# Performance work log

Hardware: AMD Instinct MI355X
Metric: run time of the kernel (lower is better)

The kernel has to match this reference:

```python
import jax, jax.numpy as jnp
import numpy as np


def setup_inputs() -> dict:
    key = jax.random.key(0)
    k_x, k_g, k_fc, k_pj = jax.random.split(key, 4)
    B, T, C, H, E = 4, 2048, 1024, 2048, 8
    n_layer = 12
    x = jax.random.normal(k_x, (B, T, C), dtype=jnp.float32)
    w_gate = 0.02 * jax.random.normal(k_g, (C, E), dtype=jnp.float32)
    w_fc = 0.02 * jax.random.normal(k_fc, (C, H, E), dtype=jnp.float32)
    w_proj = (0.02 * (2 * n_layer) ** -0.5) * jax.random.normal(k_pj, (H, C, E), dtype=jnp.float32)
    return {"x": x, "w_gate": w_gate, "w_fc": w_fc, "w_proj": w_proj, "top_k": 2}


def reference(x, w_gate, w_fc, w_proj, top_k):
    # x: (B,T,C); w_gate: (C,E); w_fc: (C,H,E); w_proj: (H,C,E)
    E = w_gate.shape[-1]
    gate = jnp.einsum('btc,ce->bte', x, w_gate)                  # gating logits
    top_vals, top_idx = jax.lax.top_k(gate, top_k)               # (B,T,K) — raw logits used as combine weights (as in source)
    # Per-expert combine weight: sum_k top_val_k * onehot(idx_k) — zero for unselected experts.
    # This is mathematically identical to gathering the K expert weight slices per token
    # (the source's gather+einsum) but avoids the (B,T,C,H,K) weight blowup.
    onehot = jax.nn.one_hot(top_idx, E, dtype=x.dtype)           # (B,T,K,E)
    w_e = jnp.einsum('btk,btke->bte', top_vals, onehot)          # (B,T,E)
    h = jax.nn.silu(jnp.einsum('btc,che->bthe', x, w_fc))        # (B,T,H,E)
    o = jnp.einsum('bthe,bte,hce->btc', h, w_e, w_proj)          # weighted expert combine
    return o
```

## Files before the change

### kernel.cpp

```cpp
#include <hip/hip_runtime.h>
#include <hip/hip_bf16.h>


#define NTOK 8192
#define CD   1024
#define HD   2048
#define NE   8
#define NSLOT 16384
#define MTILES 20
#define BK   64
#define NT1  (CD / BK)
#define NT2  (HD / BK)
#define PACK_BLOCKS 2048

typedef short  short4_t  __attribute__((ext_vector_type(4)));
typedef short  short8_t  __attribute__((ext_vector_type(8)));
typedef __bf16 bf16x8_t  __attribute__((ext_vector_type(8)));
typedef float  f32x4_t   __attribute__((ext_vector_type(4)));

struct FragArg {
  short8_t v;
  __device__ operator short8_t() const { return v; }
  __device__ operator bf16x8_t() const { return __builtin_bit_cast(bf16x8_t, v); }
};

static __device__ __forceinline__ float b2f(unsigned short u) {
  union { float f; unsigned int i; } w; w.i = ((unsigned int)u) << 16; return w.f;
}
static __device__ __forceinline__ unsigned short f2b(float f) {
  unsigned int u = __float_as_uint(f);
  u += 0x7fffu + ((u >> 16) & 1u);
  return (unsigned short)(u >> 16);
}
static __device__ __forceinline__ void gl2lds16(const void* g, void* l) {
  __builtin_amdgcn_global_load_lds((__attribute__((address_space(1))) void*)g,
                                   (__attribute__((address_space(3))) void*)l,
                                   16, 0, 0);
}

static __device__ __forceinline__ void pack_tile(
    const float* __restrict__ in, unsigned short* __restrict__ out,
    int D0, int D1, int b0, int b1, unsigned short* smem, int t)
{
  int d1i = t & 31, d0q = t >> 5;
  #pragma unroll
  for (int r = 0; r < 4; ++r) {
    int d0i = d0q * 4 + r;
    const float* src = in + ((size_t)(b0 + d0i) * D1 + (b1 + d1i)) * NE;
    float4 v0 = *(const float4*)src;
    float4 v1 = *(const float4*)(src + 4);
    unsigned short* dst0 = &smem[d1i * 40 + d0i];
    dst0[0 * 32 * 40] = f2b(v0.x);
    dst0[1 * 32 * 40] = f2b(v0.y);
    dst0[2 * 32 * 40] = f2b(v0.z);
    dst0[3 * 32 * 40] = f2b(v0.w);
    dst0[4 * 32 * 40] = f2b(v1.x);
    dst0[5 * 32 * 40] = f2b(v1.y);
    dst0[6 * 32 * 40] = f2b(v1.z);
    dst0[7 * 32 * 40] = f2b(v1.w);
  }
  __syncthreads();
  int dchunk = t & 3, d1w = (t >> 2) & 31, ehalf = t >> 7;
  #pragma unroll
  for (int p = 0; p < 4; ++p) {
    int e = ehalf + 2 * p;
    short8_t v = *(const short8_t*)&smem[e * 32 * 40 + d1w * 40 + dchunk * 8];
    *(short8_t*)(out + ((size_t)e * D1 + (b1 + d1w)) * D0 + b0 + dchunk * 8) = v;
  }
}

#define GATE_BLOCKS (NTOK / 4)
__global__ __launch_bounds__(256) void prep_kernel(
    const float* __restrict__ x, const float* __restrict__ wg,
    const float* __restrict__ wfc,
    unsigned short* __restrict__ xb, unsigned short* __restrict__ wfcp,
    int* __restrict__ tok_e, float* __restrict__ tok_v,
    int* __restrict__ g_counts)
{
  __shared__ __align__(16) unsigned short lds[NE * 32 * 40];
  __shared__ int hist[NE];
  int t = threadIdx.x;

  if (blockIdx.x < GATE_BLOCKS) {
    if (t < NE) hist[t] = 0;
    __syncthreads();
    int wv = t >> 6, lane = t & 63;
    int tk = blockIdx.x * 4 + wv;
    const float* xr = x + (size_t)tk * CD;
    unsigned short* xbr = xb + (size_t)tk * CD;
    float acc[NE] = {0, 0, 0, 0, 0, 0, 0, 0};
    #pragma unroll
    for (int jj = 0; jj < 4; ++jj) {
      int c0 = (lane + 64 * jj) * 4;
      float4 xv = *(const float4*)(xr + c0);
      short4_t ob;
      ob[0] = (short)f2b(xv.x); ob[1] = (short)f2b(xv.y);
      ob[2] = (short)f2b(xv.z); ob[3] = (short)f2b(xv.w);
      *(short4_t*)(xbr + c0) = ob;
      #pragma unroll
      for (int j = 0; j < 4; ++j) {
        float xf = (j == 0) ? xv.x : (j == 1) ? xv.y : (j == 2) ? xv.z : xv.w;
        const float* wr = wg + (size_t)(c0 + j) * NE;
        float4 w0 = *(const float4*)wr;
        float4 w1 = *(const float4*)(wr + 4);
        acc[0] += xf * w0.x; acc[1] += xf * w0.y;
        acc[2] += xf * w0.z; acc[3] += xf * w0.w;
        acc[4] += xf * w1.x; acc[5] += xf * w1.y;
        acc[6] += xf * w1.z; acc[7] += xf * w1.w;
      }
    }
    #pragma unroll
    for (int off = 32; off >= 1; off >>= 1)
      #pragma unroll
      for (int e = 0; e < NE; ++e) acc[e] += __shfl_down(acc[e], off, 64);
    if (lane == 0) {
      float v1 = -3.0e38f, v2 = -3.0e38f; int i1 = 0, i2 = 1;
      #pragma unroll
      for (int e = 0; e < NE; ++e) {
        float g = acc[e];
        if (g > v1) { v2 = v1; i2 = i1; v1 = g; i1 = e; }
        else if (g > v2) { v2 = g; i2 = e; }
      }
      tok_e[tk * 2] = i1; tok_e[tk * 2 + 1] = i2;
      tok_v[tk * 2] = v1; tok_v[tk * 2 + 1] = v2;
      atomicAdd(&hist[i1], 1); atomicAdd(&hist[i2], 1);
    }
    __syncthreads();
    if (t < NE && hist[t] > 0) atomicAdd(&g_counts[t], hist[t]);
  } else {
    int pid = blockIdx.x - GATE_BLOCKS;
    int bx = pid & 63, by = pid >> 6;
    pack_tile(wfc, wfcp, CD, HD, by * 32, bx * 32, lds, t);
  }
}

__global__ __launch_bounds__(256) void scatter_kernel(
    const int* __restrict__ tok_e, const float* __restrict__ tok_v,
    const int* __restrict__ g_counts, int* __restrict__ g_cursor,
    int* __restrict__ g_base,
    int* __restrict__ bucket_tok, float* __restrict__ bucket_v,
    int* __restrict__ slot_of)
{
  int gid = blockIdx.x * 256 + threadIdx.x;
  int lane = threadIdx.x & 63;
  int base[NE];
  { int o = 0;
    #pragma unroll
    for (int e = 0; e < NE; ++e) { base[e] = o; o += g_counts[e]; } }
  int e = tok_e[gid];
  unsigned long long lanebit = 1ull << lane;
  int pos = 0;
  #pragma unroll
  for (int ee = 0; ee < NE; ++ee) {
    unsigned long long m = __ballot(e == ee);
    if (e == ee) {
      int leader = __ffsll((long long)m) - 1;
      int cnt = __popcll(m);
      int start = 0;
      if (lane == leader) start = atomicAdd(&g_cursor[ee], cnt);
      start = __shfl(start, leader, 64);
      pos = start + __popcll(m & (lanebit - 1));
    }
  }
  int sl = base[e] + pos;
  bucket_tok[sl] = gid >> 1;
  bucket_v[sl]   = tok_v[gid];
  slot_of[gid]   = sl;
  if (gid < NE) g_base[gid] = base[gid];
}

__global__ __launch_bounds__(256, 2) void gemm1_kernel(
    const unsigned short* __restrict__ xb, const unsigned short* __restrict__ wfcp,
    const float* __restrict__ wpj, unsigned short* __restrict__ wpjp,
    const int* __restrict__ g_counts, const int* __restrict__ g_base,
    const int* __restrict__ bucket_tok, const float* __restrict__ bucket_v,
    unsigned short* __restrict__ hbuf)
{
  __shared__ __align__(16) unsigned short smem[2][2][2][128][32];
  __shared__ int   s_tok[128];
  __shared__ float s_v[128];
  int t = threadIdx.x;

  if (blockIdx.x < PACK_BLOCKS) {
    int pid = blockIdx.x;
    int bx = pid & 63, by = pid >> 6;
    pack_tile(wpj, wpjp, HD, CD, bx * 32, by * 32, &smem[0][0][0][0][0], t);
    return;
  }

  int id = blockIdx.x - PACK_BLOCKS;
  int e = id & 7;
  int r = id >> 3;
  int nt = r & 15;
  int mt = r >> 4;

  int cnt = g_counts[e];
  int m0 = mt * 128;
  if (m0 >= cnt) return;
  int base = g_base[e];
  int n0 = nt * 128;

  if (t < 128) {
    int ok = (m0 + t) < cnt;
    s_tok[t] = ok ? bucket_tok[base + m0 + t] : 0;
    s_v[t]   = ok ? bucket_v[base + m0 + t] : 0.0f;
  }
  __syncthreads();

  int lane = t & 63, wv = t >> 6;
  int srow = t >> 2;
  int spc  = t & 3;
  int sw   = (spc ^ (srow & 3)) * 8;
  const unsigned short* aS0 = xb + (size_t)s_tok[srow] * CD + sw;
  const unsigned short* aS1 = xb + (size_t)s_tok[srow + 64] * CD + sw;
  const unsigned short* bS0 = wfcp + ((size_t)e * HD + n0 + srow) * CD + sw;
  const unsigned short* bS1 = wfcp + ((size_t)e * HD + n0 + srow + 64) * CD + sw;

  #define STG1(tt, kh) do {                                              \
    int _ko = (tt) * BK + (kh) * 32;                                     \
    int _b  = (tt) & 1;                                                  \
    gl2lds16(aS0 + _ko, &smem[0][_b][kh][wv * 16][0]);                   \
    gl2lds16(aS1 + _ko, &smem[0][_b][kh][64 + wv * 16][0]);              \
    gl2lds16(bS0 + _ko, &smem[1][_b][kh][wv * 16][0]);                   \
    gl2lds16(bS1 + _ko, &smem[1][_b][kh][64 + wv * 16][0]);              \
  } while (0)

  int wm = (wv & 1) * 64, wn = (wv >> 1) * 64;
  int ml = lane & 15, kq = lane >> 4;
  int sw8 = (kq ^ (ml & 3)) * 8;

  f32x4_t acc[4][4];
  #pragma unroll
  for (int i = 0; i < 4; ++i)
    #pragma unroll
    for (int j = 0; j < 4; ++j) acc[i][j] = (f32x4_t){0.f, 0.f, 0.f, 0.f};

  STG1(0, 0); STG1(0, 1); STG1(1, 0);
  asm volatile("s_waitcnt vmcnt(8)" ::: "memory");
  __builtin_amdgcn_s_barrier();
  asm volatile("" ::: "memory");

  #pragma unroll 1
  for (int tt = 0; tt < NT1; ++tt) {
    int buf = tt & 1;
    short8_t af[4], bfr[4];
    #pragma unroll
    for (int i = 0; i < 4; ++i) {
      af[i]  = *(const short8_t*)&smem[0][buf][0][wm + i * 16 + ml][sw8];
      bfr[i] = *(const short8_t*)&smem[1][buf][0][wn + i * 16 + ml][sw8];
    }
    if (tt + 1 < NT1) STG1(tt + 1, 1);
    __builtin_amdgcn_s_barrier();
    __builtin_amdgcn_s_setprio(1);
    #pragma unroll
    for (int i = 0; i < 4; ++i)
      #pragma unroll
      for (int j = 0; j < 4; ++j)
        acc[i][j] = __builtin_amdgcn_mfma_f32_16x16x32_bf16(
            FragArg{af[i]}, FragArg{bfr[j]}, acc[i][j], 0, 0, 0);
    __builtin_amdgcn_s_setprio(0);
    if (tt < NT1 - 1) asm volatile("s_waitcnt vmcnt(8)" ::: "memory");
    else              asm volatile("s_waitcnt vmcnt(0)" ::: "memory");
    __builtin_amdgcn_s_barrier();
    asm volatile("" ::: "memory");
    #pragma unroll
    for (int i = 0; i < 4; ++i) {
      af[i]  = *(const short8_t*)&smem[0][buf][1][wm + i * 16 + ml][sw8];
      bfr[i] = *(const short8_t*)&smem[1][buf][1][wn + i * 16 + ml][sw8];
    }
    if (tt + 2 < NT1) STG1(tt + 2, 0);
    __builtin_amdgcn_s_barrier();
    __builtin_amdgcn_s_setprio(1);
    #pragma unroll
    for (int i = 0; i < 4; ++i)
      #pragma unroll
      for (int j = 0; j < 4; ++j)
        acc[i][j] = __builtin_amdgcn_mfma_f32_16x16x32_bf16(
            FragArg{af[i]}, FragArg{bfr[j]}, acc[i][j], 0, 0, 0);
    __builtin_amdgcn_s_setprio(0);
    if (tt + 2 < NT1)      asm volatile("s_waitcnt vmcnt(8)" ::: "memory");
    else if (tt + 1 < NT1) asm volatile("s_waitcnt vmcnt(4)" ::: "memory");
    __builtin_amdgcn_s_barrier();
    asm volatile("" ::: "memory");
  }
  #undef STG1

  #pragma unroll
  for (int i = 0; i < 4; ++i) {
    int rb = wm + i * 16 + kq * 4;
    #pragma unroll
    for (int r2 = 0; r2 < 4; ++r2) {
      int row = rb + r2;
      if (m0 + row < cnt) {
        float v = s_v[row];
        size_t ro = (size_t)(base + m0 + row) * HD + n0;
        #pragma unroll
        for (int j = 0; j < 4; ++j) {
          float z = acc[i][j][r2];
          float val = v * (z / (1.0f + __expf(-z)));
          hbuf[ro + wn + j * 16 + ml] = f2b(val);
        }
      }
    }
  }
}

__global__ __launch_bounds__(256, 2) void gemm2_kernel(
    const unsigned short* __restrict__ hbuf, const unsigned short* __restrict__ wpjp,
    const int* __restrict__ g_counts, const int* __restrict__ g_base,
    unsigned short* __restrict__ oslot)
{
  __shared__ __align__(16) unsigned short smem[2][2][2][128][32];

  int id = blockIdx.x;
  int e = id & 7;
  int r = id >> 3;
  int nt = r & 7;
  int mt = r >> 3;

  int cnt = g_counts[e];
  int m0 = mt * 128;
  if (m0 >= cnt) return;
  int base = g_base[e];
  int n0 = nt * 128;

  int t = threadIdx.x;
  int lane = t & 63, wv = t >> 6;
  int srow = t >> 2;
  int spc  = t & 3;
  int sw   = (spc ^ (srow & 3)) * 8;
  const unsigned short* aS0 = hbuf + ((size_t)(base + m0 + srow)) * HD + sw;
  const unsigned short* aS1 = hbuf + ((size_t)(base + m0 + srow + 64)) * HD + sw;
  const unsigned short* bS0 = wpjp + ((size_t)e * CD + n0 + srow) * HD + sw;
  const unsigned short* bS1 = wpjp + ((size_t)e * CD + n0 + srow + 64) * HD + sw;

  #define STG2(tt, kh) do {                                              \
    int _ko = (tt) * BK + (kh) * 32;                                     \
    int _b  = (tt) & 1;                                                  \
    gl2lds16(aS0 + _ko, &smem[0][_b][kh][wv * 16][0]);                   \
    gl2lds16(aS1 + _ko, &smem[0][_b][kh][64 + wv * 16][0]);              \
    gl2lds16(bS0 + _ko, &smem[1][_b][kh][wv * 16][0]);                   \
    gl2lds16(bS1 + _ko, &smem[1][_b][kh][64 + wv * 16][0]);              \
  } while (0)

  int wm = (wv & 1) * 64, wn = (wv >> 1) * 64;
  int ml = lane & 15, kq = lane >> 4;
  int sw8 = (kq ^ (ml & 3)) * 8;

  f32x4_t acc[4][4];
  #pragma unroll
  for (int i = 0; i < 4; ++i)
    #pragma unroll
    for (int j = 0; j < 4; ++j) acc[i][j] = (f32x4_t){0.f, 0.f, 0.f, 0.f};

  asm volatile("s_waitcnt vmcnt(0)" ::: "memory");
  STG2(0, 0); STG2(0, 1); STG2(1, 0);
  asm volatile("s_waitcnt vmcnt(8)" ::: "memory");
  __builtin_amdgcn_s_barrier();
  asm volatile("" ::: "memory");

  #pragma unroll 1
  for (int tt = 0; tt < NT2; ++tt) {
    int buf = tt & 1;
    short8_t af[4], bfr[4];
    #pragma unroll
    for (int i = 0; i < 4; ++i) {
      af[i]  = *(const short8_t*)&smem[0][buf][0][wm + i * 16 + ml][sw8];
      bfr[i] = *(const short8_t*)&smem[1][buf][0][wn + i * 16 + ml][sw8];
    }
    if (tt + 1 < NT2) STG2(tt + 1, 1);
    __builtin_amdgcn_s_barrier();
    __builtin_amdgcn_s_setprio(1);
    #pragma unroll
    for (int i = 0; i < 4; ++i)
      #pragma unroll
      for (int j = 0; j < 4; ++j)
        acc[i][j] = __builtin_amdgcn_mfma_f32_16x16x32_bf16(
            FragArg{af[i]}, FragArg{bfr[j]}, acc[i][j], 0, 0, 0);
    __builtin_amdgcn_s_setprio(0);
    if (tt < NT2 - 1) asm volatile("s_waitcnt vmcnt(8)" ::: "memory");
    else              asm volatile("s_waitcnt vmcnt(0)" ::: "memory");
    __builtin_amdgcn_s_barrier();
    asm volatile("" ::: "memory");
    #pragma unroll
    for (int i = 0; i < 4; ++i) {
      af[i]  = *(const short8_t*)&smem[0][buf][1][wm + i * 16 + ml][sw8];
      bfr[i] = *(const short8_t*)&smem[1][buf][1][wn + i * 16 + ml][sw8];
    }
    if (tt + 2 < NT2) STG2(tt + 2, 0);
    __builtin_amdgcn_s_barrier();
    __builtin_amdgcn_s_setprio(1);
    #pragma unroll
    for (int i = 0; i < 4; ++i)
      #pragma unroll
      for (int j = 0; j < 4; ++j)
        acc[i][j] = __builtin_amdgcn_mfma_f32_16x16x32_bf16(
            FragArg{af[i]}, FragArg{bfr[j]}, acc[i][j], 0, 0, 0);
    __builtin_amdgcn_s_setprio(0);
    if (tt + 2 < NT2)      asm volatile("s_waitcnt vmcnt(8)" ::: "memory");
    else if (tt + 1 < NT2) asm volatile("s_waitcnt vmcnt(4)" ::: "memory");
    __builtin_amdgcn_s_barrier();
    asm volatile("" ::: "memory");
  }
  #undef STG2

  #pragma unroll
  for (int i = 0; i < 4; ++i) {
    int rb = wm + i * 16 + kq * 4;
    #pragma unroll
    for (int r2 = 0; r2 < 4; ++r2) {
      int row = rb + r2;
      if (m0 + row < cnt) {
        size_t ro = (size_t)(base + m0 + row) * CD + n0;
        #pragma unroll
        for (int j = 0; j < 4; ++j)
          oslot[ro + wn + j * 16 + ml] = f2b(acc[i][j][r2]);
      }
    }
  }
}

__global__ __launch_bounds__(256) void combine_kernel(
    const unsigned short* __restrict__ oslot, const int* __restrict__ slot_of,
    float* __restrict__ out)
{
  int gid = blockIdx.x * 256 + threadIdx.x;
  int tk = gid >> 7;
  int ch = (gid & 127) * 8;
  int s0 = slot_of[tk * 2], s1 = slot_of[tk * 2 + 1];
  short8_t a = *(const short8_t*)(oslot + (size_t)s0 * CD + ch);
  short8_t b = *(const short8_t*)(oslot + (size_t)s1 * CD + ch);
  float* op = out + (size_t)tk * CD + ch;
  float4 o0, o1;
  o0.x = b2f((unsigned short)a[0]) + b2f((unsigned short)b[0]);
  o0.y = b2f((unsigned short)a[1]) + b2f((unsigned short)b[1]);
  o0.z = b2f((unsigned short)a[2]) + b2f((unsigned short)b[2]);
  o0.w = b2f((unsigned short)a[3]) + b2f((unsigned short)b[3]);
  o1.x = b2f((unsigned short)a[4]) + b2f((unsigned short)b[4]);
  o1.y = b2f((unsigned short)a[5]) + b2f((unsigned short)b[5]);
  o1.z = b2f((unsigned short)a[6]) + b2f((unsigned short)b[6]);
  o1.w = b2f((unsigned short)a[7]) + b2f((unsigned short)b[7]);
  *(float4*)op = o0;
  *(float4*)(op + 4) = o1;
}

extern "C" void kernel_launch(void* const* d_in, const int* in_sizes, int n_in,
                              void* d_out, int out_size, void* d_ws, size_t ws_size,
                              hipStream_t stream)
{
  const float* x   = (const float*)d_in[0];
  const float* wg  = (const float*)d_in[1];
  const float* wfc = (const float*)d_in[2];
  const float* wpj = (const float*)d_in[3];
  float* out = (float*)d_out;

  char* w = (char*)d_ws;
  unsigned short* wfcp  = (unsigned short*)w; w += (size_t)NE * HD * CD * 2;
  unsigned short* wpjp  = (unsigned short*)w; w += (size_t)NE * CD * HD * 2;
  unsigned short* xb    = (unsigned short*)w; w += (size_t)NTOK * CD * 2;
  unsigned short* hbuf  = (unsigned short*)w; w += (size_t)NSLOT * HD * 2;
  unsigned short* oslot = (unsigned short*)w; w += (size_t)NSLOT * CD * 2;
  int*   tok_e      = (int*)w;   w += NSLOT * 4;
  float* tok_v      = (float*)w; w += NSLOT * 4;
  int*   slot_of    = (int*)w;   w += NSLOT * 4;
  int*   bucket_tok = (int*)w;   w += NSLOT * 4;
  float* bucket_v   = (float*)w; w += NSLOT * 4;
  int*   g_counts   = (int*)w;   w += NE * 4;
  int*   g_cursor   = (int*)w;   w += NE * 4;
  int*   g_base     = (int*)w;   w += 256;

  hipMemsetAsync(g_counts, 0, 2 * NE * sizeof(int), stream);
  prep_kernel<<<GATE_BLOCKS + PACK_BLOCKS, 256, 0, stream>>>(
      x, wg, wfc, xb, wfcp, tok_e, tok_v, g_counts);
  scatter_kernel<<<NSLOT / 256, 256, 0, stream>>>(
      tok_e, tok_v, g_counts, g_cursor, g_base, bucket_tok, bucket_v, slot_of);
  gemm1_kernel<<<PACK_BLOCKS + (HD / 128) * MTILES * NE, 256, 0, stream>>>(
      xb, wfcp, wpj, wpjp, g_counts, g_base, bucket_tok, bucket_v, hbuf);
  gemm2_kernel<<<(CD / 128) * MTILES * NE, 256, 0, stream>>>(
      hbuf, wpjp, g_counts, g_base, oslot);
  combine_kernel<<<(NTOK * CD / 8) / 256, 256, 0, stream>>>(oslot, slot_of, out);
}
```

Before: 447.0 us.

## Enlarge grouped GEMM tiles to 256x256 with 8 waves; move w_proj packing to prep

```diff
diff --git a/kernel.cpp b/kernel.cpp
--- a/kernel.cpp
+++ b/kernel.cpp
@@ -7,7 +7,7 @@
 #define HD   2048
 #define NE   8
 #define NSLOT 16384
-#define MTILES 20
+#define MT256 10
 #define BK   64
 #define NT1  (CD / BK)
 #define NT2  (HD / BK)
@@ -72,8 +72,9 @@
 #define GATE_BLOCKS (NTOK / 4)
 __global__ __launch_bounds__(256) void prep_kernel(
     const float* __restrict__ x, const float* __restrict__ wg,
-    const float* __restrict__ wfc,
+    const float* __restrict__ wfc, const float* __restrict__ wpj,
     unsigned short* __restrict__ xb, unsigned short* __restrict__ wfcp,
+    unsigned short* __restrict__ wpjp,
     int* __restrict__ tok_e, float* __restrict__ tok_v,
     int* __restrict__ g_counts)
 {
@@ -127,10 +128,14 @@
     }
     __syncthreads();
     if (t < NE && hist[t] > 0) atomicAdd(&g_counts[t], hist[t]);
-  } else {
+  } else if (blockIdx.x < GATE_BLOCKS + PACK_BLOCKS) {
     int pid = blockIdx.x - GATE_BLOCKS;
     int bx = pid & 63, by = pid >> 6;
     pack_tile(wfc, wfcp, CD, HD, by * 32, bx * 32, lds, t);
+  } else {
+    int pid = blockIdx.x - GATE_BLOCKS - PACK_BLOCKS;
+    int bx = pid & 63, by = pid >> 6;
+    pack_tile(wpj, wpjp, HD, CD, bx * 32, by * 32, lds, t);
   }
 }
 
@@ -169,69 +174,63 @@
   if (gid < NE) g_base[gid] = base[gid];
 }
 
-__global__ __launch_bounds__(256, 2) void gemm1_kernel(
+__global__ __launch_bounds__(512, 2) void gemm1_kernel(
     const unsigned short* __restrict__ xb, const unsigned short* __restrict__ wfcp,
-    const float* __restrict__ wpj, unsigned short* __restrict__ wpjp,
     const int* __restrict__ g_counts, const int* __restrict__ g_base,
     const int* __restrict__ bucket_tok, const float* __restrict__ bucket_v,
     unsigned short* __restrict__ hbuf)
 {
-  __shared__ __align__(16) unsigned short smem[2][2][2][128][32];
-  __shared__ int   s_tok[128];
-  __shared__ float s_v[128];
-  int t = threadIdx.x;
-
-  if (blockIdx.x < PACK_BLOCKS) {
-    int pid = blockIdx.x;
-    int bx = pid & 63, by = pid >> 6;
-    pack_tile(wpj, wpjp, HD, CD, bx * 32, by * 32, &smem[0][0][0][0][0], t);
-    return;
-  }
-
-  int id = blockIdx.x - PACK_BLOCKS;
+  __shared__ __align__(16) unsigned short lsA[2][2][256][32];
+  __shared__ __align__(16) unsigned short lsB[2][2][256][32];
+  __shared__ int   s_tok[256];
+  __shared__ float s_v[256];
+
+  int id = blockIdx.x;
   int e = id & 7;
   int r = id >> 3;
-  int nt = r & 15;
-  int mt = r >> 4;
+  int nt = r & 7;
+  int mt = r >> 3;
 
   int cnt = g_counts[e];
-  int m0 = mt * 128;
+  int m0 = mt * 256;
   if (m0 >= cnt) return;
   int base = g_base[e];
-  int n0 = nt * 128;
-
-  if (t < 128) {
+  int n0 = nt * 256;
+
+  int t = threadIdx.x;
+  if (t < 256) {
     int ok = (m0 + t) < cnt;
     s_tok[t] = ok ? bucket_tok[base + m0 + t] : 0;
     s_v[t]   = ok ? bucket_v[base + m0 + t] : 0.0f;
   }
   __syncthreads();
 
-  int lane = t & 63, wv = t >> 6;
-  int srow = t >> 2;
-  int spc  = t & 3;
-  int sw   = (spc ^ (srow & 3)) * 8;
-  const unsigned short* aS0 = xb + (size_t)s_tok[srow] * CD + sw;
-  const unsigned short* aS1 = xb + (size_t)s_tok[srow + 64] * CD + sw;
-  const unsigned short* bS0 = wfcp + ((size_t)e * HD + n0 + srow) * CD + sw;
-  const unsigned short* bS1 = wfcp + ((size_t)e * HD + n0 + srow + 64) * CD + sw;
+  int lane = t & 63, w = t >> 6;
+  int w32 = w * 32;
+  int rl0 = w32 + (lane >> 2);
+  int rl1 = rl0 + 16;
+  int cb  = ((lane & 3) ^ (rl0 & 3)) * 8;
+  const unsigned short* aS0 = xb + (size_t)s_tok[rl0] * CD + cb;
+  const unsigned short* aS1 = xb + (size_t)s_tok[rl1] * CD + cb;
+  const unsigned short* bS0 = wfcp + ((size_t)e * HD + n0 + rl0) * CD + cb;
+  const unsigned short* bS1 = wfcp + ((size_t)e * HD + n0 + rl1) * CD + cb;
 
   #define STG1(tt, kh) do {                                              \
     int _ko = (tt) * BK + (kh) * 32;                                     \
     int _b  = (tt) & 1;                                                  \
-    gl2lds16(aS0 + _ko, &smem[0][_b][kh][wv * 16][0]);                   \
-    gl2lds16(aS1 + _ko, &smem[0][_b][kh][64 + wv * 16][0]);              \
-    gl2lds16(bS0 + _ko, &smem[1][_b][kh][wv * 16][0]);                   \
-    gl2lds16(bS1 + _ko, &smem[1][_b][kh][64 + wv * 16][0]);              \
+    gl2lds16(aS0 + _ko, &lsA[_b][kh][w32][0]);                           \
+    gl2lds16(aS1 + _ko, &lsA[_b][kh][w32 + 16][0]);                      \
+    gl2lds16(bS0 + _ko, &lsB[_b][kh][w32][0]);                           \
+    gl2lds16(bS1 + _ko, &lsB[_b][kh][w32 + 16][0]);                      \
   } while (0)
 
-  int wm = (wv & 1) * 64, wn = (wv >> 1) * 64;
+  int wr = w >> 2, wc = w & 3;
   int ml = lane & 15, kq = lane >> 4;
   int sw8 = (kq ^ (ml & 3)) * 8;
 
-  f32x4_t acc[4][4];
-  #pragma unroll
-  for (int i = 0; i < 4; ++i)
+  f32x4_t acc[8][4];
+  #pragma unroll
+  for (int i = 0; i < 8; ++i)
     #pragma unroll
     for (int j = 0; j < 4; ++j) acc[i][j] = (f32x4_t){0.f, 0.f, 0.f, 0.f};
 
@@ -243,17 +242,18 @@
   #pragma unroll 1
   for (int tt = 0; tt < NT1; ++tt) {
     int buf = tt & 1;
-    short8_t af[4], bfr[4];
-    #pragma unroll
-    for (int i = 0; i < 4; ++i) {
-      af[i]  = *(const short8_t*)&smem[0][buf][0][wm + i * 16 + ml][sw8];
-      bfr[i] = *(const short8_t*)&smem[1][buf][0][wn + i * 16 + ml][sw8];
-    }
+    short8_t af[8], bfr[4];
+    #pragma unroll
+    for (int i = 0; i < 8; ++i)
+      af[i]  = *(const short8_t*)&lsA[buf][0][wr * 128 + i * 16 + ml][sw8];
+    #pragma unroll
+    for (int j = 0; j < 4; ++j)
+      bfr[j] = *(const short8_t*)&lsB[buf][0][wc * 64 + j * 16 + ml][sw8];
     if (tt + 1 < NT1) STG1(tt + 1, 1);
     __builtin_amdgcn_s_barrier();
     __builtin_amdgcn_s_setprio(1);
     #pragma unroll
-    for (int i = 0; i < 4; ++i)
+    for (int i = 0; i < 8; ++i)
       #pragma unroll
       for (int j = 0; j < 4; ++j)
         acc[i][j] = __builtin_amdgcn_mfma_f32_16x16x32_bf16(
@@ -264,15 +264,16 @@
     __builtin_amdgcn_s_barrier();
     asm volatile("" ::: "memory");
     #pragma unroll
-    for (int i = 0; i < 4; ++i) {
-      af[i]  = *(const short8_t*)&smem[0][buf][1][wm + i * 16 + ml][sw8];
-      bfr[i] = *(const short8_t*)&smem[1][buf][1][wn + i * 16 + ml][sw8];
-    }
+    for (int i = 0; i < 8; ++i)
+      af[i]  = *(const short8_t*)&lsA[buf][1][wr * 128 + i * 16 + ml][sw8];
+    #pragma unroll
+    for (int j = 0; j < 4; ++j)
+      bfr[j] = *(const short8_t*)&lsB[buf][1][wc * 64 + j * 16 + ml][sw8];
     if (tt + 2 < NT1) STG1(tt + 2, 0);
     __builtin_amdgcn_s_barrier();
     __builtin_amdgcn_s_setprio(1);
     #pragma unroll
-    for (int i = 0; i < 4; ++i)
+    for (int i = 0; i < 8; ++i)
       #pragma unroll
       for (int j = 0; j < 4; ++j)
         acc[i][j] = __builtin_amdgcn_mfma_f32_16x16x32_bf16(
@@ -286,8 +287,8 @@
   #undef STG1
 
   #pragma unroll
-  for (int i = 0; i < 4; ++i) {
-    int rb = wm + i * 16 + kq * 4;
+  for (int i = 0; i < 8; ++i) {
+    int rb = wr * 128 + i * 16 + kq * 4;
     #pragma unroll
     for (int r2 = 0; r2 < 4; ++r2) {
       int row = rb + r2;
@@ -298,58 +299,60 @@
         for (int j = 0; j < 4; ++j) {
           float z = acc[i][j][r2];
           float val = v * (z / (1.0f + __expf(-z)));
-          hbuf[ro + wn + j * 16 + ml] = f2b(val);
+          hbuf[ro + wc * 64 + j * 16 + ml] = f2b(val);
         }
       }
     }
   }
 }
 
-__global__ __launch_bounds__(256, 2) void gemm2_kernel(
+__global__ __launch_bounds__(512, 2) void gemm2_kernel(
     const unsigned short* __restrict__ hbuf, const unsigned short* __restrict__ wpjp,
     const int* __restrict__ g_counts, const int* __restrict__ g_base,
     unsigned short* __restrict__ oslot)
 {
-  __shared__ __align__(16) unsigned short smem[2][2][2][128][32];
+  __shared__ __align__(16) unsigned short lsA[2][2][256][32];
+  __shared__ __align__(16) unsigned short lsB[2][2][256][32];
 
   int id = blockIdx.x;
   int e = id & 7;
   int r = id >> 3;
-  int nt = r & 7;
-  int mt = r >> 3;
+  int nt = r & 3;
+  int mt = r >> 2;
 
   int cnt = g_counts[e];
-  int m0 = mt * 128;
+  int m0 = mt * 256;
   if (m0 >= cnt) return;
   int base = g_base[e];
-  int n0 = nt * 128;
+  int n0 = nt * 256;
 
   int t = threadIdx.x;
-  int lane = t & 63, wv = t >> 6;
-  int srow = t >> 2;
-  int spc  = t & 3;
-  int sw   = (spc ^ (srow & 3)) * 8;
-  const unsigned short* aS0 = hbuf + ((size_t)(base + m0 + srow)) * HD + sw;
-  const unsigned short* aS1 = hbuf + ((size_t)(base + m0 + srow + 64)) * HD + sw;
-  const unsigned short* bS0 = wpjp + ((size_t)e * CD + n0 + srow) * HD + sw;
-  const unsigned short* bS1 = wpjp + ((size_t)e * CD + n0 + srow + 64) * HD + sw;
+  int lane = t & 63, w = t >> 6;
+  int w32 = w * 32;
+  int rl0 = w32 + (lane >> 2);
+  int rl1 = rl0 + 16;
+  int cb  = ((lane & 3) ^ (rl0 & 3)) * 8;
+  const unsigned short* aS0 = hbuf + ((size_t)(base + m0 + rl0)) * HD + cb;
+  const unsigned short* aS1 = hbuf + ((size_t)(base + m0 + rl1)) * HD + cb;
+  const unsigned short* bS0 = wpjp + ((size_t)e * CD + n0 + rl0) * HD + cb;
+  const unsigned short* bS1 = wpjp + ((size_t)e * CD + n0 + rl1) * HD + cb;
 
   #define STG2(tt, kh) do {                                              \
     int _ko = (tt) * BK + (kh) * 32;                                     \
     int _b  = (tt) & 1;                                                  \
-    gl2lds16(aS0 + _ko, &smem[0][_b][kh][wv * 16][0]);                   \
-    gl2lds16(aS1 + _ko, &smem[0][_b][kh][64 + wv * 16][0]);              \
-    gl2lds16(bS0 + _ko, &smem[1][_b][kh][wv * 16][0]);                   \
-    gl2lds16(bS1 + _ko, &smem[1][_b][kh][64 + wv * 16][0]);              \
+    gl2lds16(aS0 + _ko, &lsA[_b][kh][w32][0]);                           \
+    gl2lds16(aS1 + _ko, &lsA[_b][kh][w32 + 16][0]);                      \
+    gl2lds16(bS0 + _ko, &lsB[_b][kh][w32][0]);                           \
+    gl2lds16(bS1 + _ko, &lsB[_b][kh][w32 + 16][0]);                      \
   } while (0)
 
-  int wm = (wv & 1) * 64, wn = (wv >> 1) * 64;
+  int wr = w >> 2, wc = w & 3;
   int ml = lane & 15, kq = lane >> 4;
   int sw8 = (kq ^ (ml & 3)) * 8;
 
-  f32x4_t acc[4][4];
-  #pragma unroll
-  for (int i = 0; i < 4; ++i)
+  f32x4_t acc[8][4];
+  #pragma unroll
+  for (int i = 0; i < 8; ++i)
     #pragma unroll
     for (int j = 0; j < 4; ++j) acc[i][j] = (f32x4_t){0.f, 0.f, 0.f, 0.f};
 
@@ -362,17 +365,18 @@
   #pragma unroll 1
   for (int tt = 0; tt < NT2; ++tt) {
     int buf = tt & 1;
-    short8_t af[4], bfr[4];
-    #pragma unroll
-    for (int i = 0; i < 4; ++i) {
-      af[i]  = *(const short8_t*)&smem[0][buf][0][wm + i * 16 + ml][sw8];
-      bfr[i] = *(const short8_t*)&smem[1][buf][0][wn + i * 16 + ml][sw8];
-    }
+    short8_t af[8], bfr[4];
+    #pragma unroll
+    for (int i = 0; i < 8; ++i)
+      af[i]  = *(const short8_t*)&lsA[buf][0][wr * 128 + i * 16 + ml][sw8];
+    #pragma unroll
+    for (int j = 0; j < 4; ++j)
+      bfr[j] = *(const short8_t*)&lsB[buf][0][wc * 64 + j * 16 + ml][sw8];
     if (tt + 1 < NT2) STG2(tt + 1, 1);
     __builtin_amdgcn_s_barrier();
     __builtin_amdgcn_s_setprio(1);
     #pragma unroll
-    for (int i = 0; i < 4; ++i)
+    for (int i = 0; i < 8; ++i)
       #pragma unroll
       for (int j = 0; j < 4; ++j)
         acc[i][j] = __builtin_amdgcn_mfma_f32_16x16x32_bf16(
@@ -383,15 +387,16 @@
     __builtin_amdgcn_s_barrier();
     asm volatile("" ::: "memory");
     #pragma unroll
-    for (int i = 0; i < 4; ++i) {
-      af[i]  = *(const short8_t*)&smem[0][buf][1][wm + i * 16 + ml][sw8];
-      bfr[i] = *(const short8_t*)&smem[1][buf][1][wn + i * 16 + ml][sw8];
-    }
+    for (int i = 0; i < 8; ++i)
+      af[i]  = *(const short8_t*)&lsA[buf][1][wr * 128 + i * 16 + ml][sw8];
+    #pragma unroll
+    for (int j = 0; j < 4; ++j)
+      bfr[j] = *(const short8_t*)&lsB[buf][1][wc * 64 + j * 16 + ml][sw8];
     if (tt + 2 < NT2) STG2(tt + 2, 0);
     __builtin_amdgcn_s_barrier();
     __builtin_amdgcn_s_setprio(1);
     #pragma unroll
-    for (int i = 0; i < 4; ++i)
+    for (int i = 0; i < 8; ++i)
       #pragma unroll
       for (int j = 0; j < 4; ++j)
         acc[i][j] = __builtin_amdgcn_mfma_f32_16x16x32_bf16(
@@ -405,8 +410,8 @@
   #undef STG2
 
   #pragma unroll
-  for (int i = 0; i < 4; ++i) {
-    int rb = wm + i * 16 + kq * 4;
+  for (int i = 0; i < 8; ++i) {
+    int rb = wr * 128 + i * 16 + kq * 4;
     #pragma unroll
     for (int r2 = 0; r2 < 4; ++r2) {
       int row = rb + r2;
@@ -414,7 +419,7 @@
         size_t ro = (size_t)(base + m0 + row) * CD + n0;
         #pragma unroll
         for (int j = 0; j < 4; ++j)
-          oslot[ro + wn + j * 16 + ml] = f2b(acc[i][j][r2]);
+          oslot[ro + wc * 64 + j * 16 + ml] = f2b(acc[i][j][r2]);
       }
     }
   }
@@ -470,13 +475,13 @@
   int*   g_base     = (int*)w;   w += 256;
 
   hipMemsetAsync(g_counts, 0, 2 * NE * sizeof(int), stream);
-  prep_kernel<<<GATE_BLOCKS + PACK_BLOCKS, 256, 0, stream>>>(
-      x, wg, wfc, xb, wfcp, tok_e, tok_v, g_counts);
+  prep_kernel<<<GATE_BLOCKS + 2 * PACK_BLOCKS, 256, 0, stream>>>(
+      x, wg, wfc, wpj, xb, wfcp, wpjp, tok_e, tok_v, g_counts);
   scatter_kernel<<<NSLOT / 256, 256, 0, stream>>>(
       tok_e, tok_v, g_counts, g_cursor, g_base, bucket_tok, bucket_v, slot_of);
-  gemm1_kernel<<<PACK_BLOCKS + (HD / 128) * MTILES * NE, 256, 0, stream>>>(
-      xb, wfcp, wpj, wpjp, g_counts, g_base, bucket_tok, bucket_v, hbuf);
-  gemm2_kernel<<<(CD / 128) * MTILES * NE, 256, 0, stream>>>(
+  gemm1_kernel<<<(HD / 256) * MT256 * NE, 512, 0, stream>>>(
+      xb, wfcp, g_counts, g_base, bucket_tok, bucket_v, hbuf);
+  gemm2_kernel<<<(CD / 256) * MT256 * NE, 512, 0, stream>>>(
       hbuf, wpjp, g_counts, g_base, oslot);
   combine_kernel<<<(NTOK * CD / 8) / 256, 256, 0, stream>>>(oslot, slot_of, out);
 }
```

Result: slower. 493.9 us (+10.5%).
